# Kernel tuning notes

Hardware: AMD Instinct MI355X
Metric: run time of the kernel (lower is better)

The kernel has to match this reference:

```python
import jax, jax.numpy as jnp
import numpy as np

B, C, P, T = 16, 128, 512, 32
H = 2
D = C // H  # 64
SCALE = D ** -0.5  # note: original scales by d^-0.5, NOT (d*t)^-0.5


def setup_inputs() -> dict:
    key = jax.random.key(0)
    kx, kw, kb = jax.random.split(key, 3)
    x = jax.random.normal(kx, (B, C, P, T), dtype=jnp.float32)
    # Conv2d(C, 3C, kernel=1) == per-pixel linear: W:[3C, C], b:[3C]
    W = jax.random.normal(kw, (3 * C, C), dtype=jnp.float32) * (C ** -0.5)
    b = jax.random.normal(kb, (3 * C,), dtype=jnp.float32) * 0.01
    return {"x": x, "W": W, "b": b}


def reference(x, W, b):
    # 1x1 conv -> pointwise channel mix
    qkv = jnp.einsum('bcpt,oc->bopt', x, W) + b[None, :, None, None]  # [B,3C,P,T]
    qkv = qkv.reshape(B, 3, H, D, P, T)
    q, k, v = qkv[:, 0], qkv[:, 1], qkv[:, 2]  # each [B,H,D,P,T]
    # flatten (d t) as feature dim, tokens along P
    q = q.transpose(0, 1, 3, 2, 4).reshape(B, H, P, D * T)
    k = k.transpose(0, 1, 3, 2, 4).reshape(B, H, P, D * T)
    v = v.transpose(0, 1, 3, 2, 4).reshape(B, H, P, D * T)
    dots = jnp.einsum('bhpe,bhqe->bhpq', q, k) * SCALE  # [B,H,P,P]
    attn = jax.nn.softmax(dots, axis=-1)
    out = jnp.einsum('bhpq,bhqe->bhpe', attn, v)  # [B,H,P,D*T]
    # b h p (d t) -> b (h d) p t
    out = out.reshape(B, H, P, D, T).transpose(0, 1, 3, 2, 4).reshape(B, C, P, T)
    return out
```

## Files before the change

### kernel.cpp

```cpp
#include <hip/hip_runtime.h>

#define BB 16
#define CC 128
#define PP 512
#define TT 32
#define HH 2
#define DD 64
#define EE 2048
#define NPIX 16384
#define SCALE 0.125f

typedef _Float16 f16_t;
typedef _Float16 f16x8_t __attribute__((ext_vector_type(8)));
typedef _Float16 f16x4_t __attribute__((ext_vector_type(4)));
typedef float    f32x4_t __attribute__((ext_vector_type(4)));

#define AS_GLOBAL __attribute__((address_space(1)))
#define AS_LDS    __attribute__((address_space(3)))

__device__ __forceinline__ void async_ld16(const void* g, void* l) {
    __builtin_amdgcn_global_load_lds((const AS_GLOBAL void*)g,
                                     (AS_LDS void*)l, 16, 0, 0);
}

__device__ __forceinline__ void gemm_lds_bt(const f16_t* __restrict__ A, int lda,
                                            const f16_t* __restrict__ Bt, int ldb,
                                            int K, int m0, int n0,
                                            f16_t* As, f16_t* Bs,
                                            f32x4_t acc[4][4])
{
    const int tid  = threadIdx.x;
    const int lane = tid & 63;
    const int wave = tid >> 6;
    const int wm = wave & 1, wn = wave >> 1;
    const int quad = lane >> 4, l16 = lane & 15;

    const f16_t* gA0 = A  + (size_t)(m0 + lane)      * lda + wave * 8;
    const f16_t* gA1 = A  + (size_t)(m0 + 64 + lane) * lda + wave * 8;
    const f16_t* gB0 = Bt + (size_t)(n0 + lane)      * ldb + wave * 8;
    const f16_t* gB1 = Bt + (size_t)(n0 + 64 + lane) * ldb + wave * 8;
    f16_t* lA0 = As + (size_t)(wave * 128)      * 8;
    f16_t* lA1 = As + (size_t)(wave * 128 + 64) * 8;
    f16_t* lB0 = Bs + (size_t)(wave * 128)      * 8;
    f16_t* lB1 = Bs + (size_t)(wave * 128 + 64) * 8;

    const int ar = wm * 64 + l16;
    const int br = wn * 64 + l16;

    for (int k0 = 0; k0 < K; k0 += 32) {
        if (k0) __syncthreads();
        async_ld16(gA0 + k0, lA0);
        async_ld16(gA1 + k0, lA1);
        async_ld16(gB0 + k0, lB0);
        async_ld16(gB1 + k0, lB1);
        __syncthreads();

        f16x8_t af[4], bf[4];
#pragma unroll
        for (int mi = 0; mi < 4; ++mi)
            af[mi] = *(const f16x8_t*)(As + (size_t)(quad * 128 + ar + mi * 16) * 8);
#pragma unroll
        for (int ni = 0; ni < 4; ++ni)
            bf[ni] = *(const f16x8_t*)(Bs + (size_t)(quad * 128 + br + ni * 16) * 8);
#pragma unroll
        for (int mi = 0; mi < 4; ++mi)
#pragma unroll
            for (int ni = 0; ni < 4; ++ni)
                acc[mi][ni] = __builtin_amdgcn_mfma_f32_16x16x32_f16(
                    af[mi], bf[ni], acc[mi][ni], 0, 0, 0);
    }
}

__global__ __launch_bounds__(256) void wcvt_kernel(const float* __restrict__ W,
                                                   f16_t* __restrict__ Wh)
{
    const int i = (blockIdx.x * 256 + threadIdx.x) * 4;
    const float4 wv = *(const float4*)(W + i);
    f16x4_t t;
    t[0] = (_Float16)wv.x; t[1] = (_Float16)wv.y;
    t[2] = (_Float16)wv.z; t[3] = (_Float16)wv.w;
    *(f16x4_t*)(Wh + i) = t;
}

__global__ __launch_bounds__(256) void proj_kernel(const float* __restrict__ x,
                                                   const f16_t* __restrict__ Wh,
                                                   const float* __restrict__ bias,
                                                   f16_t* __restrict__ q,
                                                   f16_t* __restrict__ k,
                                                   f16_t* __restrict__ v)
{
    __shared__ f16_t xs[CC * 128];
    const int b    = blockIdx.y;
    const int pt   = blockIdx.x;
    const int tid  = threadIdx.x;
    const int lane = tid & 63;
    const int wave = tid >> 6;
    const int wm   = wave & 1, wn = wave >> 1;
    const int quad = lane >> 4, l16 = lane & 15;
    const int pixb = pt * 128;

    const float* xb = x + (size_t)b * CC * NPIX;

#pragma unroll 2
    for (int r = 0; r < 8; ++r) {
        const int u  = r * 4 + wave;
        const int c0 = (u >> 1) * 8;
        const int pl = (u & 1) * 64 + lane;
        const float* g = xb + (size_t)c0 * NPIX + pixb + pl;
        float vv[8];
#pragma unroll
        for (int j = 0; j < 8; ++j) vv[j] = g[(size_t)j * NPIX];
        f16x8_t t;
#pragma unroll
        for (int j = 0; j < 8; ++j) t[j] = (_Float16)vv[j];
        *(f16x8_t*)((char*)xs + pl * 256 + ((c0 * 2) ^ ((pl & 15) << 4))) = t;
    }
    __syncthreads();

    for (int s = 0; s < 3; ++s) {
        f32x4_t acc[4][4];
#pragma unroll
        for (int i = 0; i < 4; ++i)
#pragma unroll
            for (int j = 0; j < 4; ++j) acc[i][j] = (f32x4_t){0.f, 0.f, 0.f, 0.f};

#pragma unroll
        for (int k0 = 0; k0 < CC; k0 += 32) {
            const int kq = k0 + quad * 8;
            f16x8_t af[4], bf[4];
#pragma unroll
            for (int mi = 0; mi < 4; ++mi) {
                const int o = s * 128 + wm * 64 + mi * 16 + l16;
                af[mi] = *(const f16x8_t*)(Wh + (size_t)o * CC + kq);
            }
#pragma unroll
            for (int ni = 0; ni < 4; ++ni) {
                const int pl = wn * 64 + ni * 16 + l16;
                bf[ni] = *(const f16x8_t*)((char*)xs + pl * 256 +
                                           ((kq * 2) ^ ((pl & 15) << 4)));
            }
#pragma unroll
            for (int mi = 0; mi < 4; ++mi)
#pragma unroll
                for (int ni = 0; ni < 4; ++ni)
                    acc[mi][ni] = __builtin_amdgcn_mfma_f32_16x16x32_f16(
                        af[mi], bf[ni], acc[mi][ni], 0, 0, 0);
        }

        f16_t* dst = (s == 0) ? q : (s == 1) ? k : v;
#pragma unroll
        for (int mi = 0; mi < 4; ++mi) {
#pragma unroll
            for (int r = 0; r < 4; ++r) {
                const int o_loc = wm * 64 + mi * 16 + quad * 4 + r;
                const int o     = s * 128 + o_loc;
                const float bv  = bias[o];
                const int h = o_loc >> 6, d = o_loc & 63;
#pragma unroll
                for (int ni = 0; ni < 4; ++ni) {
                    const int pix = pixb + wn * 64 + ni * 16 + l16;
                    const int p = pix >> 5, t = pix & 31;
                    const size_t addr =
                        ((size_t)((b * HH + h) * PP + p)) * EE + d * TT + t;
                    dst[addr] = (_Float16)(acc[mi][ni][r] + bv);
                }
            }
        }
    }
}

__global__ __launch_bounds__(256) void vpose_kernel(const f16_t* __restrict__ v,
                                                    f16_t* __restrict__ vt)
{
    __shared__ unsigned short lds[64][65];
    const int bh   = blockIdx.y;
    const int tile = blockIdx.x;
    const int e0 = (tile & 31) * 64;
    const int p0 = (tile >> 5) * 64;
    const int tid = threadIdx.x;
    const int r0 = tid >> 6;
    const int cc = tid & 63;
    const f16_t* vb  = v  + (size_t)bh * PP * EE;
    f16_t*       vtb = vt + (size_t)bh * EE * PP;
#pragma unroll
    for (int it = 0; it < 16; ++it) {
        const int pl = it * 4 + r0;
        lds[pl][cc] = __builtin_bit_cast(unsigned short,
                          vb[(size_t)(p0 + pl) * EE + e0 + cc]);
    }
    __syncthreads();
#pragma unroll
    for (int it = 0; it < 16; ++it) {
        const int el = it * 4 + r0;
        vtb[(size_t)(e0 + el) * PP + p0 + cc] =
            __builtin_bit_cast(_Float16, lds[cc][el]);
    }
}

__global__ __launch_bounds__(256) void qk_kernel(const f16_t* __restrict__ q,
                                                 const f16_t* __restrict__ k,
                                                 float* __restrict__ S)
{
    __shared__ f16_t As[128 * 32];
    __shared__ f16_t Bs[128 * 32];
    const int id = blockIdx.x;
    const int bh = id & 31;
    const int tile = id >> 5;
    const int mt = tile & 3, nt = tile >> 2;
    const int tid  = threadIdx.x;
    const int lane = tid & 63;
    const int wave = tid >> 6;
    const int wm = wave & 1, wn = wave >> 1;
    const int quad = lane >> 4, l16 = lane & 15;

    f32x4_t acc[4][4];
#pragma unroll
    for (int i = 0; i < 4; ++i)
#pragma unroll
        for (int j = 0; j < 4; ++j) acc[i][j] = (f32x4_t){0.f, 0.f, 0.f, 0.f};

    const f16_t* qb = q + (size_t)bh * PP * EE;
    const f16_t* kb = k + (size_t)bh * PP * EE;
    gemm_lds_bt(qb, EE, kb, EE, EE, mt * 128, nt * 128, As, Bs, acc);

    float* Sb = S + (size_t)bh * PP * PP;
#pragma unroll
    for (int mi = 0; mi < 4; ++mi)
#pragma unroll
        for (int r = 0; r < 4; ++r) {
            const int row = mt * 128 + wm * 64 + mi * 16 + quad * 4 + r;
#pragma unroll
            for (int ni = 0; ni < 4; ++ni) {
                const int col = nt * 128 + wn * 64 + ni * 16 + l16;
                Sb[(size_t)row * PP + col] = acc[mi][ni][r] * SCALE;
            }
        }
}

__global__ __launch_bounds__(256) void softmax_kernel(float* __restrict__ S)
{
    const int tid  = threadIdx.x;
    const int wave = tid >> 6;
    const int lane = tid & 63;
    const int row  = blockIdx.x * 4 + wave;
    float* rp = S + (size_t)row * PP;

    const float4 a = *(const float4*)(rp + lane * 8);
    const float4 b = *(const float4*)(rp + lane * 8 + 4);

    float m = fmaxf(fmaxf(fmaxf(a.x, a.y), fmaxf(a.z, a.w)),
                    fmaxf(fmaxf(b.x, b.y), fmaxf(b.z, b.w)));
#pragma unroll
    for (int off = 1; off < 64; off <<= 1) m = fmaxf(m, __shfl_xor(m, off, 64));

    float e[8];
    e[0] = expf(a.x - m); e[1] = expf(a.y - m);
    e[2] = expf(a.z - m); e[3] = expf(a.w - m);
    e[4] = expf(b.x - m); e[5] = expf(b.y - m);
    e[6] = expf(b.z - m); e[7] = expf(b.w - m);

    float sum = e[0] + e[1] + e[2] + e[3] + e[4] + e[5] + e[6] + e[7];
#pragma unroll
    for (int off = 1; off < 64; off <<= 1) sum += __shfl_xor(sum, off, 64);
    const float inv = 1.0f / sum;

    __syncthreads();

    f16_t* prow = (f16_t*)rp;
    f16x8_t o;
#pragma unroll
    for (int j = 0; j < 8; ++j) o[j] = (_Float16)(e[j] * inv);
    *(f16x8_t*)(prow + lane * 8) = o;
}

__global__ __launch_bounds__(256) void pv_kernel(const f16_t* __restrict__ Pm,
                                                 const f16_t* __restrict__ vt,
                                                 float* __restrict__ out)
{
    __shared__ f16_t As[128 * 32];
    __shared__ f16_t Bs[128 * 32];
    const int id = blockIdx.x;
    const int bh = id & 31;
    const int tile = id >> 5;
    const int mt = tile & 3, nt = tile >> 2;
    const int tid  = threadIdx.x;
    const int lane = tid & 63;
    const int wave = tid >> 6;
    const int wm = wave & 1, wn = wave >> 1;
    const int quad = lane >> 4, l16 = lane & 15;

    f32x4_t acc[4][4];
#pragma unroll
    for (int i = 0; i < 4; ++i)
#pragma unroll
        for (int j = 0; j < 4; ++j) acc[i][j] = (f32x4_t){0.f, 0.f, 0.f, 0.f};

    const f16_t* Pb  = Pm + (size_t)bh * PP * 1024;
    const f16_t* vtb = vt + (size_t)bh * EE * PP;
    gemm_lds_bt(Pb, 1024, vtb, PP, PP, mt * 128, nt * 128, As, Bs, acc);

    const int b = bh >> 1, h = bh & 1;
#pragma unroll
    for (int mi = 0; mi < 4; ++mi)
#pragma unroll
        for (int r = 0; r < 4; ++r) {
            const int p = mt * 128 + wm * 64 + mi * 16 + quad * 4 + r;
#pragma unroll
            for (int ni = 0; ni < 4; ++ni) {
                const int e = nt * 128 + wn * 64 + ni * 16 + l16;
                const int d = e >> 5, t = e & 31;
                out[(((size_t)(b * CC + h * DD + d)) * PP + p) * TT + t] =
                    acc[mi][ni][r];
            }
        }
}

extern "C" void kernel_launch(void* const* d_in, const int* in_sizes, int n_in,
                              void* d_out, int out_size, void* d_ws, size_t ws_size,
                              hipStream_t stream)
{
    const float* x    = (const float*)d_in[0];
    const float* W    = (const float*)d_in[1];
    const float* bias = (const float*)d_in[2];
    float* out = (float*)d_out;

    char* ws = (char*)d_ws;
    const size_t MiB = 1024ull * 1024ull;
    f16_t* q  = (f16_t*)(ws);
    f16_t* k  = (f16_t*)(ws + 64 * MiB);
    f16_t* v  = (f16_t*)(ws + 128 * MiB);
    f16_t* vt = (f16_t*)(ws + 192 * MiB);
    float* S  = (float*)(ws + 256 * MiB);
    f16_t* Wh = (f16_t*)(ws + 256 * MiB);

    wcvt_kernel<<<dim3(48), dim3(256), 0, stream>>>(W, Wh);
    proj_kernel<<<dim3(128, 16), dim3(256), 0, stream>>>(x, Wh, bias, q, k, v);
    vpose_kernel<<<dim3(256, 32), dim3(256), 0, stream>>>(v, vt);
    qk_kernel<<<dim3(512), dim3(256), 0, stream>>>(q, k, S);
    softmax_kernel<<<dim3(4096), dim3(256), 0, stream>>>(S);
    pv_kernel<<<dim3(2048), dim3(256), 0, stream>>>((const f16_t*)S, vt, out);
}
```

Measured before the change: 510.2 us.

## Double-buffer GEMM LDS tiles with BK=64 and vectorize V transpose

The shared GEMM helper becomes a templated double-buffered loop with a K-tile of 64. It issues async global-to-LDS loads for the next tile while MFMAs run on the current one, removing one barrier per step and hiding load latency in the QK and PV kernels. The V transpose kernel now uses 16-byte vector global loads and stores instead of scalar half loads. The trade-off is that LDS per block grows from 16KB to 64KB, which lowers occupancy, and the column reads in the transpose may cause LDS bank conflicts.

```diff
diff --git a/kernel.cpp b/kernel.cpp
--- a/kernel.cpp
+++ b/kernel.cpp
@@ -23,11 +23,12 @@
                                      (AS_LDS void*)l, 16, 0, 0);
 }
 
-__device__ __forceinline__ void gemm_lds_bt(const f16_t* __restrict__ A, int lda,
-                                            const f16_t* __restrict__ Bt, int ldb,
-                                            int K, int m0, int n0,
-                                            f16_t* As, f16_t* Bs,
-                                            f32x4_t acc[4][4])
+template<int BK>
+__device__ __forceinline__ void gemm_lds_bt_db(const f16_t* __restrict__ A, int lda,
+                                               const f16_t* __restrict__ Bt, int ldb,
+                                               int K, int m0, int n0,
+                                               f16_t* As, f16_t* Bs,
+                                               f32x4_t acc[4][4])
 {
     const int tid  = threadIdx.x;
     const int lane = tid & 63;
@@ -35,39 +36,59 @@
     const int wm = wave & 1, wn = wave >> 1;
     const int quad = lane >> 4, l16 = lane & 15;
 
-    const f16_t* gA0 = A  + (size_t)(m0 + lane)      * lda + wave * 8;
-    const f16_t* gA1 = A  + (size_t)(m0 + 64 + lane) * lda + wave * 8;
-    const f16_t* gB0 = Bt + (size_t)(n0 + lane)      * ldb + wave * 8;
-    const f16_t* gB1 = Bt + (size_t)(n0 + 64 + lane) * ldb + wave * 8;
-    f16_t* lA0 = As + (size_t)(wave * 128)      * 8;
-    f16_t* lA1 = As + (size_t)(wave * 128 + 64) * 8;
-    f16_t* lB0 = Bs + (size_t)(wave * 128)      * 8;
-    f16_t* lB1 = Bs + (size_t)(wave * 128 + 64) * 8;
+    constexpr int NCH  = BK / 8;
+    constexpr int CPW  = NCH / 4;
+    constexpr int TILE = 128 * BK;
 
     const int ar = wm * 64 + l16;
     const int br = wn * 64 + l16;
 
-    for (int k0 = 0; k0 < K; k0 += 32) {
-        if (k0) __syncthreads();
-        async_ld16(gA0 + k0, lA0);
-        async_ld16(gA1 + k0, lA1);
-        async_ld16(gB0 + k0, lB0);
-        async_ld16(gB1 + k0, lB1);
+    auto stage = [&](int buf, int k0) {
+        f16_t* dA = As + buf * TILE;
+        f16_t* dB = Bs + buf * TILE;
+#pragma unroll
+        for (int cc = 0; cc < CPW; ++cc) {
+            const int ch = wave * CPW + cc;
+            const int kk = k0 + ch * 8;
+            async_ld16(A  + (size_t)(m0 + lane)      * lda + kk,
+                       dA + (size_t)(ch * 128)       * 8);
+            async_ld16(A  + (size_t)(m0 + 64 + lane) * lda + kk,
+                       dA + (size_t)(ch * 128 + 64)  * 8);
+            async_ld16(Bt + (size_t)(n0 + lane)      * ldb + kk,
+                       dB + (size_t)(ch * 128)       * 8);
+            async_ld16(Bt + (size_t)(n0 + 64 + lane) * ldb + kk,
+                       dB + (size_t)(ch * 128 + 64)  * 8);
+        }
+    };
+
+    stage(0, 0);
+    __syncthreads();
+
+    int cur = 0;
+    for (int k0 = 0; k0 < K; k0 += BK) {
+        if (k0 + BK < K) stage(cur ^ 1, k0 + BK);
+
+        const f16_t* sA = As + cur * TILE;
+        const f16_t* sB = Bs + cur * TILE;
+#pragma unroll
+        for (int kk = 0; kk < BK / 32; ++kk) {
+            const int chq = kk * 4 + quad;
+            f16x8_t af[4], bf[4];
+#pragma unroll
+            for (int mi = 0; mi < 4; ++mi)
+                af[mi] = *(const f16x8_t*)(sA + (size_t)(chq * 128 + ar + mi * 16) * 8);
+#pragma unroll
+            for (int ni = 0; ni < 4; ++ni)
+                bf[ni] = *(const f16x8_t*)(sB + (size_t)(chq * 128 + br + ni * 16) * 8);
+#pragma unroll
+            for (int mi = 0; mi < 4; ++mi)
+#pragma unroll
+                for (int ni = 0; ni < 4; ++ni)
+                    acc[mi][ni] = __builtin_amdgcn_mfma_f32_16x16x32_f16(
+                        af[mi], bf[ni], acc[mi][ni], 0, 0, 0);
+        }
         __syncthreads();
-
-        f16x8_t af[4], bf[4];
-#pragma unroll
-        for (int mi = 0; mi < 4; ++mi)
-            af[mi] = *(const f16x8_t*)(As + (size_t)(quad * 128 + ar + mi * 16) * 8);
-#pragma unroll
-        for (int ni = 0; ni < 4; ++ni)
-            bf[ni] = *(const f16x8_t*)(Bs + (size_t)(quad * 128 + br + ni * 16) * 8);
-#pragma unroll
-        for (int mi = 0; mi < 4; ++mi)
-#pragma unroll
-            for (int ni = 0; ni < 4; ++ni)
-                acc[mi][ni] = __builtin_amdgcn_mfma_f32_16x16x32_f16(
-                    af[mi], bf[ni], acc[mi][ni], 0, 0, 0);
+        cur ^= 1;
     }
 }
 
@@ -178,22 +199,27 @@
     const int e0 = (tile & 31) * 64;
     const int p0 = (tile >> 5) * 64;
     const int tid = threadIdx.x;
-    const int r0 = tid >> 6;
-    const int cc = tid & 63;
+    const int rw  = tid >> 3;
+    const int c8  = (tid & 7) * 8;
     const f16_t* vb  = v  + (size_t)bh * PP * EE;
     f16_t*       vtb = vt + (size_t)bh * EE * PP;
 #pragma unroll
-    for (int it = 0; it < 16; ++it) {
-        const int pl = it * 4 + r0;
-        lds[pl][cc] = __builtin_bit_cast(unsigned short,
-                          vb[(size_t)(p0 + pl) * EE + e0 + cc]);
+    for (int half = 0; half < 2; ++half) {
+        const int p = rw + half * 32;
+        const f16x8_t t = *(const f16x8_t*)(vb + (size_t)(p0 + p) * EE + e0 + c8);
+#pragma unroll
+        for (int j = 0; j < 8; ++j)
+            lds[p][c8 + j] = __builtin_bit_cast(unsigned short, (_Float16)t[j]);
     }
     __syncthreads();
 #pragma unroll
-    for (int it = 0; it < 16; ++it) {
-        const int el = it * 4 + r0;
-        vtb[(size_t)(e0 + el) * PP + p0 + cc] =
-            __builtin_bit_cast(_Float16, lds[cc][el]);
+    for (int half = 0; half < 2; ++half) {
+        const int e = rw + half * 32;
+        f16x8_t t;
+#pragma unroll
+        for (int j = 0; j < 8; ++j)
+            t[j] = __builtin_bit_cast(_Float16, lds[c8 + j][e]);
+        *(f16x8_t*)(vtb + (size_t)(e0 + e) * PP + p0 + c8) = t;
     }
 }
 
@@ -201,8 +227,8 @@
                                                  const f16_t* __restrict__ k,
                                                  float* __restrict__ S)
 {
-    __shared__ f16_t As[128 * 32];
-    __shared__ f16_t Bs[128 * 32];
+    __shared__ f16_t As[2 * 128 * 64];
+    __shared__ f16_t Bs[2 * 128 * 64];
     const int id = blockIdx.x;
     const int bh = id & 31;
     const int tile = id >> 5;
@@ -221,7 +247,7 @@
 
     const f16_t* qb = q + (size_t)bh * PP * EE;
     const f16_t* kb = k + (size_t)bh * PP * EE;
-    gemm_lds_bt(qb, EE, kb, EE, EE, mt * 128, nt * 128, As, Bs, acc);
+    gemm_lds_bt_db<64>(qb, EE, kb, EE, EE, mt * 128, nt * 128, As, Bs, acc);
 
     float* Sb = S + (size_t)bh * PP * PP;
 #pragma unroll
@@ -277,8 +303,8 @@
                                                  const f16_t* __restrict__ vt,
                                                  float* __restrict__ out)
 {
-    __shared__ f16_t As[128 * 32];
-    __shared__ f16_t Bs[128 * 32];
+    __shared__ f16_t As[2 * 128 * 64];
+    __shared__ f16_t Bs[2 * 128 * 64];
     const int id = blockIdx.x;
     const int bh = id & 31;
     const int tile = id >> 5;
@@ -297,7 +323,7 @@
 
     const f16_t* Pb  = Pm + (size_t)bh * PP * 1024;
     const f16_t* vtb = vt + (size_t)bh * EE * PP;
-    gemm_lds_bt(Pb, 1024, vtb, PP, PP, mt * 128, nt * 128, As, Bs, acc);
+    gemm_lds_bt_db<64>(Pb, 1024, vtb, PP, PP, mt * 128, nt * 128, As, Bs, acc);
 
     const int b = bh >> 1, h = bh & 1;
 #pragma unroll
```

Measured after the change: 523.0 us. 2.5% more time.

## Swap GEMM operand roles so epilogue stores vectorize; vectorize V transpose

Applied to the files above, without the earlier changes.

In the QKV projection and PV kernels, the MFMA operand roles are swapped: pixels or embedding become the M dimension. Each lane's four accumulator rows are then contiguous in the output's t axis and can be written as one 4-wide vector store instead of scalar stores. The V transpose kernel now reads and writes 8-wide f16 vectors instead of scalar halves. This targets the uncoalesced scalar global writes in the epilogues, at the cost of LDS bank conflicts in the transpose's column-wise reads.

```diff
diff --git a/kernel.cpp b/kernel.cpp
--- a/kernel.cpp
+++ b/kernel.cpp
@@ -127,43 +127,47 @@
 #pragma unroll
         for (int k0 = 0; k0 < CC; k0 += 32) {
             const int kq = k0 + quad * 8;
-            f16x8_t af[4], bf[4];
+            f16x8_t xf[4], wf[4];
 #pragma unroll
             for (int mi = 0; mi < 4; ++mi) {
-                const int o = s * 128 + wm * 64 + mi * 16 + l16;
-                af[mi] = *(const f16x8_t*)(Wh + (size_t)o * CC + kq);
-            }
-#pragma unroll
-            for (int ni = 0; ni < 4; ++ni) {
-                const int pl = wn * 64 + ni * 16 + l16;
-                bf[ni] = *(const f16x8_t*)((char*)xs + pl * 256 +
+                const int pl = wm * 64 + mi * 16 + l16;
+                xf[mi] = *(const f16x8_t*)((char*)xs + pl * 256 +
                                            ((kq * 2) ^ ((pl & 15) << 4)));
             }
 #pragma unroll
+            for (int ni = 0; ni < 4; ++ni) {
+                const int o = s * 128 + wn * 64 + ni * 16 + l16;
+                wf[ni] = *(const f16x8_t*)(Wh + (size_t)o * CC + kq);
+            }
+#pragma unroll
             for (int mi = 0; mi < 4; ++mi)
 #pragma unroll
                 for (int ni = 0; ni < 4; ++ni)
                     acc[mi][ni] = __builtin_amdgcn_mfma_f32_16x16x32_f16(
-                        af[mi], bf[ni], acc[mi][ni], 0, 0, 0);
+                        xf[mi], wf[ni], acc[mi][ni], 0, 0, 0);
         }
 
         f16_t* dst = (s == 0) ? q : (s == 1) ? k : v;
+        float bv[4];
+#pragma unroll
+        for (int ni = 0; ni < 4; ++ni)
+            bv[ni] = bias[s * 128 + wn * 64 + ni * 16 + l16];
+
+        const int h = wn;
 #pragma unroll
         for (int mi = 0; mi < 4; ++mi) {
-#pragma unroll
-            for (int r = 0; r < 4; ++r) {
-                const int o_loc = wm * 64 + mi * 16 + quad * 4 + r;
-                const int o     = s * 128 + o_loc;
-                const float bv  = bias[o];
-                const int h = o_loc >> 6, d = o_loc & 63;
-#pragma unroll
-                for (int ni = 0; ni < 4; ++ni) {
-                    const int pix = pixb + wn * 64 + ni * 16 + l16;
-                    const int p = pix >> 5, t = pix & 31;
-                    const size_t addr =
-                        ((size_t)((b * HH + h) * PP + p)) * EE + d * TT + t;
-                    dst[addr] = (_Float16)(acc[mi][ni][r] + bv);
-                }
+            const int pix0 = pixb + wm * 64 + mi * 16 + quad * 4;
+            const int p  = pix0 >> 5;
+            const int t0 = pix0 & 31;
+#pragma unroll
+            for (int ni = 0; ni < 4; ++ni) {
+                const int d = ni * 16 + l16;
+                f16x4_t o4;
+#pragma unroll
+                for (int r = 0; r < 4; ++r)
+                    o4[r] = (_Float16)(acc[mi][ni][r] + bv[ni]);
+                *(f16x4_t*)(dst + ((size_t)((b * HH + h) * PP + p)) * EE
+                                + d * TT + t0) = o4;
             }
         }
     }
@@ -178,22 +182,27 @@
     const int e0 = (tile & 31) * 64;
     const int p0 = (tile >> 5) * 64;
     const int tid = threadIdx.x;
-    const int r0 = tid >> 6;
-    const int cc = tid & 63;
+    const int rw  = tid >> 3;
+    const int c8  = (tid & 7) * 8;
     const f16_t* vb  = v  + (size_t)bh * PP * EE;
     f16_t*       vtb = vt + (size_t)bh * EE * PP;
 #pragma unroll
-    for (int it = 0; it < 16; ++it) {
-        const int pl = it * 4 + r0;
-        lds[pl][cc] = __builtin_bit_cast(unsigned short,
-                          vb[(size_t)(p0 + pl) * EE + e0 + cc]);
+    for (int half = 0; half < 2; ++half) {
+        const int p = rw + half * 32;
+        const f16x8_t t = *(const f16x8_t*)(vb + (size_t)(p0 + p) * EE + e0 + c8);
+#pragma unroll
+        for (int j = 0; j < 8; ++j)
+            lds[p][c8 + j] = __builtin_bit_cast(unsigned short, (_Float16)t[j]);
     }
     __syncthreads();
 #pragma unroll
-    for (int it = 0; it < 16; ++it) {
-        const int el = it * 4 + r0;
-        vtb[(size_t)(e0 + el) * PP + p0 + cc] =
-            __builtin_bit_cast(_Float16, lds[cc][el]);
+    for (int half = 0; half < 2; ++half) {
+        const int e = rw + half * 32;
+        f16x8_t t;
+#pragma unroll
+        for (int j = 0; j < 8; ++j)
+            t[j] = __builtin_bit_cast(_Float16, lds[c8 + j][e]);
+        *(f16x8_t*)(vtb + (size_t)(e0 + e) * PP + p0 + c8) = t;
     }
 }
 
@@ -282,7 +291,7 @@
     const int id = blockIdx.x;
     const int bh = id & 31;
     const int tile = id >> 5;
-    const int mt = tile & 3, nt = tile >> 2;
+    const int nt = tile & 3, mt = tile >> 2;
     const int tid  = threadIdx.x;
     const int lane = tid & 63;
     const int wave = tid >> 6;
@@ -297,22 +306,21 @@
 
     const f16_t* Pb  = Pm + (size_t)bh * PP * 1024;
     const f16_t* vtb = vt + (size_t)bh * EE * PP;
-    gemm_lds_bt(Pb, 1024, vtb, PP, PP, mt * 128, nt * 128, As, Bs, acc);
+    gemm_lds_bt(vtb, PP, Pb, 1024, PP, mt * 128, nt * 128, As, Bs, acc);
 
     const int b = bh >> 1, h = bh & 1;
 #pragma unroll
-    for (int mi = 0; mi < 4; ++mi)
-#pragma unroll
-        for (int r = 0; r < 4; ++r) {
-            const int p = mt * 128 + wm * 64 + mi * 16 + quad * 4 + r;
-#pragma unroll
-            for (int ni = 0; ni < 4; ++ni) {
-                const int e = nt * 128 + wn * 64 + ni * 16 + l16;
-                const int d = e >> 5, t = e & 31;
-                out[(((size_t)(b * CC + h * DD + d)) * PP + p) * TT + t] =
-                    acc[mi][ni][r];
-            }
+    for (int mi = 0; mi < 4; ++mi) {
+        const int e0 = mt * 128 + wm * 64 + mi * 16 + quad * 4;
+        const int d  = e0 >> 5;
+        const int t0 = e0 & 31;
+#pragma unroll
+        for (int ni = 0; ni < 4; ++ni) {
+            const int p = nt * 128 + wn * 64 + ni * 16 + l16;
+            *(f32x4_t*)(out + ((size_t)(b * CC + h * DD + d) * PP + p) * TT + t0)
+                = acc[mi][ni];
         }
+    }
 }
 
 extern "C" void kernel_launch(void* const* d_in, const int* in_sizes, int n_in,
```

New measurement: 503.3 us. About the same (-1.4%).
